# Kernel optimization log

Measured on AMD Instinct MI355X. Metric: run time of the kernel, lower is better.

## Reference

```python
import jax, jax.numpy as jnp
import numpy as np

N = 20000       # nodes
E = 262144      # edges
DA, DV, DD = 128, 64, 32
R = 16          # CP rank of TensorProds
NRAD = 8        # radial basis size (hardcoded 8 in module)
R0 = 5.0        # cutoff radius r0


def setup_inputs() -> dict:
    key = jax.random.key(0)
    ks = jax.random.split(key, 13)
    nrm = lambda k, shape, fan: jax.random.normal(k, shape, jnp.float32) / np.sqrt(fan)
    return {
        'r_ij': jax.random.normal(ks[0], (E, 3), jnp.float32),
        'x_a': jax.random.normal(ks[1], (N, DA), jnp.float32),
        'x_v': jax.random.normal(ks[2], (N, DV, 3), jnp.float32),
        'x_d': jax.random.normal(ks[3], (N, DD, 3, 3), jnp.float32),
        'W1_a': nrm(ks[4], (3, R, DA), DA),   # tp_000, tp_011, tp_022 (rank-0 input)
        'W1_v': nrm(ks[5], (4, R, DV), DV),   # tp_101, tp_110, tp_112, tp_121
        'W1_d': nrm(ks[6], (4, R, DD), DD),   # tp_202, tp_211, tp_220, tp_222
        'W2': nrm(ks[7], (11, R, NRAD), NRAD),  # radial-side proj for all 11 TPs
        'Wo_a': nrm(ks[8], (3, DA, R), R),    # outputs of tp_000, tp_110, tp_220
        'Wo_v': nrm(ks[9], (4, DV, R), R),    # outputs of tp_011, tp_101, tp_121, tp_211
        'Wo_d': nrm(ks[10], (4, DD, R), R),   # outputs of tp_022, tp_112, tp_202, tp_222
        'src': jax.random.randint(ks[11], (E,), 0, N),
        'dst': jax.random.randint(ks[12], (E,), 0, N),
    }


def tens_sigmoid_vec(v, eps=1e-6):
    # direction-preserving bounded nonlinearity on rank-1 tensors
    n = jnp.linalg.norm(v, axis=-1, keepdims=True)
    return v * (2.0 * jax.nn.sigmoid(n) - 1.0) / (n + eps)


def _forward(r_ij, x_a, x_v, x_d, W1_a, W1_v, W1_d, W2, Wo_a, Wo_v, Wo_d, src, dst):
    n_nodes = x_a.shape[0]
    # radial_encode_edge(r, 8, r0)
    npi = jnp.pi * jnp.arange(NRAD, dtype=jnp.float32)
    x_sq = jnp.sum(r_ij * r_ij, -1) / R0                       # (E,)
    rad = jnp.cos(npi * jnp.sqrt(x_sq)[:, None]) * jax.nn.relu(1.0 - x_sq)[:, None]  # (E,8)
    rv = tens_sigmoid_vec(r_ij * (17.0 / R0))                  # (E,3)
    phi_a = rad                                                # (E,8)
    phi_v = rad[..., None] * rv[:, None, :]                    # (E,8,3)
    phi_d = rad[..., None, None] * rv[:, None, None, :] * rv[:, None, :, None]  # (E,8,3,3)
    # edges_read_dst: gather node features at destination nodes
    xa_j, xv_j, xd_j = x_a[dst], x_v[dst], x_d[dst]
    p1 = lambda W, x: jnp.einsum('rc,ec...->er...', W, x)      # channel->CP-rank proj
    outp = lambda Wo, t: jnp.einsum('dr,er...->ed...', Wo, t)  # CP-rank->channel proj
    p2a = lambda i: jnp.einsum('rc,ec->er', W2[i], phi_a)
    p2v = lambda i: jnp.einsum('rc,eci->eri', W2[i], phi_v)
    p2d = lambda i: jnp.einsum('rc,ecij->erij', W2[i], phi_d)
    # W2 index order: 000,110,220,011,101,121,211,022,112,202,222
    pa000, pa011, pa022 = p1(W1_a[0], xa_j), p1(W1_a[1], xa_j), p1(W1_a[2], xa_j)
    pv101, pv110, pv112, pv121 = (p1(W1_v[i], xv_j) for i in range(4))
    pd202, pd211, pd220, pd222 = (p1(W1_d[i], xd_j) for i in range(4))
    psi_a = (outp(Wo_a[0], pa000 * p2a(0))
             + outp(Wo_a[1], jnp.einsum('eri,eri->er', pv110, p2v(1)))
             + outp(Wo_a[2], jnp.einsum('erij,erij->er', pd220, p2d(2))))
    psi_v = (outp(Wo_v[0], pa011[..., None] * p2v(3))
             + outp(Wo_v[1], pv101 * p2a(4)[..., None])
             + outp(Wo_v[2], jnp.einsum('eri,erij->erj', pv121, p2d(5)))
             + outp(Wo_v[3], jnp.einsum('erij,erj->eri', pd211, p2v(6))))
    psi_d = (outp(Wo_d[0], pa022[..., None, None] * p2d(7))
             + outp(Wo_d[1], jnp.einsum('eri,erj->erij', pv112, p2v(8)))
             + outp(Wo_d[2], pd202 * p2a(9)[..., None, None])
             + outp(Wo_d[3], jnp.einsum('erik,erkj->erij', pd222, p2d(10))))
    # edges_reduce_src: scatter-add messages to source nodes
    B_a = jax.ops.segment_sum(psi_a, src, num_segments=n_nodes)
    B_v = jax.ops.segment_sum(psi_v, src, num_segments=n_nodes)
    B_d = jax.ops.segment_sum(psi_d, src, num_segments=n_nodes)
    return (B_a, B_v, B_d)


def reference(r_ij, x_a, x_v, x_d, W1_a, W1_v, W1_d, W2, Wo_a, Wo_v, Wo_d, src, dst):
    return _forward(r_ij, x_a, x_v, x_d, W1_a, W1_v, W1_d, W2, Wo_a, Wo_v, Wo_d, src, dst)
```

## Files before the change

kernel.cpp:

```cpp
#include <hip/hip_runtime.h>
#include <hip/hip_bf16.h>
#include <math.h>

#define PI_F 3.14159265358979323846f
#define R0_F 5.0f


static __device__ __forceinline__ float dot4(float4 a, float4 b) {
  return a.x * b.x + a.y * b.y + a.z * b.z + a.w * b.w;
}

__global__ __launch_bounds__(256) void node_proj_kernel(
    const float* __restrict__ x_a, const float* __restrict__ x_v, const float* __restrict__ x_d,
    const float* __restrict__ W1_a, const float* __restrict__ W1_v, const float* __restrict__ W1_d,
    float* __restrict__ P, int N)
{
  __shared__ float S[12352];
  const int tid = threadIdx.x;
  const int lane = tid & 63;
  const int wu = __builtin_amdgcn_readfirstlane(tid >> 6);
  const int n0 = blockIdx.x * 64;
  const int nrem = min(N - n0, 64);
  const int phase = blockIdx.y;

  if (phase == 0) {
    for (int idx4 = tid; idx4 < nrem * 32; idx4 += 256) {
      int n = idx4 >> 5, c4 = idx4 & 31;
      float4 v = ((const float4*)(x_a + (size_t)(n0 + n) * 128))[c4];
      float* d = &S[n * 129 + c4 * 4];
      d[0] = v.x; d[1] = v.y; d[2] = v.z; d[3] = v.w;
    }
    __syncthreads();
    float acc[12];
    #pragma unroll
    for (int q = 0; q < 12; q++) acc[q] = 0.0f;
    const float* xrow = &S[lane * 129];
    for (int c0 = 0; c0 < 128; c0 += 16) {
      float xr[16];
      #pragma unroll
      for (int j = 0; j < 16; j++) xr[j] = xrow[c0 + j];
      #pragma unroll
      for (int q = 0; q < 12; q++) {
        int o = wu * 12 + q;
        const float* wp = W1_a + (o >> 4) * 2048 + (o & 15) * 128 + c0;
        float s = 0.0f;
        #pragma unroll
        for (int j = 0; j < 16; j++) s += wp[j] * xr[j];
        acc[q] += s;
      }
    }
    __syncthreads();
    #pragma unroll
    for (int q = 0; q < 12; q++) S[lane * 49 + wu * 12 + q] = acc[q];
    __syncthreads();
    for (int u = tid; u < nrem * 12; u += 256) {
      int n = u / 12, m4 = u - n * 12;
      const float* s = &S[n * 49 + m4 * 4];
      ((float4*)(P + (size_t)(n0 + n) * 816))[m4] = make_float4(s[0], s[1], s[2], s[3]);
    }
  } else if (phase == 1) {
    for (int idx4 = tid; idx4 < nrem * 48; idx4 += 256) {
      int n = idx4 / 48, m4 = idx4 - n * 48;
      float4 v = ((const float4*)(x_v + (size_t)(n0 + n) * 192))[m4];
      float* d = &S[n * 193 + m4 * 4];
      d[0] = v.x; d[1] = v.y; d[2] = v.z; d[3] = v.w;
    }
    __syncthreads();
    float acc[16][3];
    #pragma unroll
    for (int r = 0; r < 16; r++)
      #pragma unroll
      for (int i = 0; i < 3; i++) acc[r][i] = 0.0f;
    const float* xrow = &S[lane * 193];
    for (int c0 = 0; c0 < 64; c0 += 16) {
      float xr[16][3];
      #pragma unroll
      for (int j = 0; j < 16; j++) {
        xr[j][0] = xrow[(c0 + j) * 3 + 0];
        xr[j][1] = xrow[(c0 + j) * 3 + 1];
        xr[j][2] = xrow[(c0 + j) * 3 + 2];
      }
      #pragma unroll
      for (int r = 0; r < 16; r++) {
        const float* wp = W1_v + wu * 1024 + r * 64 + c0;
        #pragma unroll
        for (int j = 0; j < 16; j++) {
          float w = wp[j];
          acc[r][0] += w * xr[j][0];
          acc[r][1] += w * xr[j][1];
          acc[r][2] += w * xr[j][2];
        }
      }
    }
    __syncthreads();
    #pragma unroll
    for (int r = 0; r < 16; r++)
      #pragma unroll
      for (int i = 0; i < 3; i++)
        S[lane * 193 + wu * 48 + r * 3 + i] = acc[r][i];
    __syncthreads();
    for (int u = tid; u < nrem * 48; u += 256) {
      int n = u / 48, m4 = u - n * 48;
      const float* s = &S[n * 193 + m4 * 4];
      ((float4*)(P + (size_t)(n0 + n) * 816 + 48))[m4] = make_float4(s[0], s[1], s[2], s[3]);
    }
  } else if (phase == 2) {
    for (int idx = tid; idx < nrem * 160; idx += 256) {
      int n = idx / 160, m = idx - n * 160, c = m / 5, ij = m - c * 5;
      S[n * 161 + m] = x_d[(size_t)(n0 + n) * 288 + c * 9 + ij];
    }
    __syncthreads();
    float acc[16][5];
    #pragma unroll
    for (int r = 0; r < 16; r++)
      #pragma unroll
      for (int t = 0; t < 5; t++) acc[r][t] = 0.0f;
    const float* xrow = &S[lane * 161];
    for (int c0 = 0; c0 < 32; c0 += 8) {
      float xr[8][5];
      #pragma unroll
      for (int j = 0; j < 8; j++)
        #pragma unroll
        for (int t = 0; t < 5; t++) xr[j][t] = xrow[(c0 + j) * 5 + t];
      #pragma unroll
      for (int r = 0; r < 16; r++) {
        const float* wp = W1_d + wu * 512 + r * 32 + c0;
        #pragma unroll
        for (int j = 0; j < 8; j++) {
          float w = wp[j];
          #pragma unroll
          for (int t = 0; t < 5; t++) acc[r][t] += w * xr[j][t];
        }
      }
    }
    #pragma unroll
    for (int h = 0; h < 2; h++) {
      __syncthreads();
      if ((lane >> 5) == h) {
        int l5 = lane & 31;
        #pragma unroll
        for (int r = 0; r < 16; r++)
          #pragma unroll
          for (int t = 0; t < 5; t++)
            S[l5 * 321 + wu * 80 + r * 5 + t] = acc[r][t];
      }
      __syncthreads();
      int nbase = h * 32;
      int cnt = min(nrem - nbase, 32);
      for (int u = tid; u < cnt * 320; u += 256) {
        int n = u / 320, m = u - n * 320;
        int kk = m / 80, mm = m - kk * 80, rr = mm / 5, t = mm - rr * 5;
        P[(size_t)(n0 + nbase + n) * 816 + 240 + kk * 144 + 9 * rr + t] = S[n * 321 + m];
      }
    }
  } else {
    for (int idx = tid; idx < nrem * 128; idx += 256) {
      int n = idx >> 7, m = idx & 127, c = m >> 2, t = m & 3;
      S[n * 129 + m] = x_d[(size_t)(n0 + n) * 288 + c * 9 + 5 + t];
    }
    __syncthreads();
    float acc[16][4];
    #pragma unroll
    for (int r = 0; r < 16; r++)
      #pragma unroll
      for (int t = 0; t < 4; t++) acc[r][t] = 0.0f;
    const float* xrow = &S[lane * 129];
    for (int c0 = 0; c0 < 32; c0 += 8) {
      float xr[8][4];
      #pragma unroll
      for (int j = 0; j < 8; j++)
        #pragma unroll
        for (int t = 0; t < 4; t++) xr[j][t] = xrow[(c0 + j) * 4 + t];
      #pragma unroll
      for (int r = 0; r < 16; r++) {
        const float* wp = W1_d + wu * 512 + r * 32 + c0;
        #pragma unroll
        for (int j = 0; j < 8; j++) {
          float w = wp[j];
          #pragma unroll
          for (int t = 0; t < 4; t++) acc[r][t] += w * xr[j][t];
        }
      }
    }
    #pragma unroll
    for (int h = 0; h < 2; h++) {
      __syncthreads();
      if ((lane >> 5) == h) {
        int l5 = lane & 31;
        #pragma unroll
        for (int r = 0; r < 16; r++)
          #pragma unroll
          for (int t = 0; t < 4; t++)
            S[l5 * 257 + wu * 64 + r * 4 + t] = acc[r][t];
      }
      __syncthreads();
      int nbase = h * 32;
      int cnt = min(nrem - nbase, 32);
      for (int u = tid; u < cnt * 256; u += 256) {
        int n = u >> 8, m = u & 255;
        int kk = m >> 6, mm = m & 63, rr = mm >> 2, t = mm & 3;
        P[(size_t)(n0 + nbase + n) * 816 + 240 + kk * 144 + 9 * rr + 5 + t] = S[n * 257 + m];
      }
    }
  }
}

__global__ void hist_kernel(const int* __restrict__ src, int* __restrict__ counts, int E) {
  int e = blockIdx.x * 256 + threadIdx.x;
  if (e < E) atomicAdd(&counts[src[e]], 1);
}

__global__ __launch_bounds__(1024) void scan_kernel(
    const int* __restrict__ counts, int* __restrict__ offs, int* __restrict__ cursor,
    int N, int E)
{
  __shared__ int part[1024];
  int tid = threadIdx.x;
  int chunk = (N + 1023) / 1024;
  int lo = tid * chunk, hi = min(lo + chunk, N);
  int s = 0;
  for (int i = lo; i < hi; i++) s += counts[i];
  part[tid] = s;
  __syncthreads();
  for (int off = 1; off < 1024; off <<= 1) {
    int v = (tid >= off) ? part[tid - off] : 0;
    __syncthreads();
    part[tid] += v;
    __syncthreads();
  }
  int run = part[tid] - s;
  for (int i = lo; i < hi; i++) { offs[i] = run; cursor[i] = run; run += counts[i]; }
  if (tid == 0) offs[N] = E;
}

__global__ void scatter_kernel(const int* __restrict__ src, int* __restrict__ cursor,
                               int* __restrict__ eidx, int E) {
  int e = blockIdx.x * 256 + threadIdx.x;
  if (e < E) { int p = atomicAdd(&cursor[src[e]], 1); eidx[p] = e; }
}

__global__ __launch_bounds__(256) void node_gather_kernel(
    const float* __restrict__ r_ij, const int* __restrict__ dst,
    const int* __restrict__ offs, const int* __restrict__ eidx,
    const float* __restrict__ Pg, const float* __restrict__ W2,
    const float* __restrict__ Wo_a, const float* __restrict__ Wo_v, const float* __restrict__ Wo_d,
    float* __restrict__ out, int N)
{
  __shared__ __align__(16) float Sall[7488];
  const int wid = threadIdx.x >> 6;
  const int lane = threadIdx.x & 63;
  const int n = blockIdx.x * 4 + wid;
  if (n >= N) return;
  float* S = Sall + wid * 1872;
  float4* S4 = (float4*)S;
  int* Si = (int*)S;
  const int off = offs[n], deg = offs[n + 1] - off;

  int aP[12], aQ[12], aF[12];
  unsigned typm = 0;
  #pragma unroll
  for (int p = 0; p < 3; p++) {
    int t = lane + 64 * p;
    int k = t / 48, m = t - 48 * k, jj = m >> 4, r = m & 15;
    int q_ = 816 + (3 + k) * 16 + r;
    int P_, F_;
    if (k == 0)      { P_ = 16 + r;              F_ = 992 + jj; }
    else if (k == 1) { P_ = 48 + 3 * r + jj;     F_ = 995; }
    else if (k == 2) { P_ = 192 + 3 * r;         F_ = 992 + jj; typm |= 1u << p; }
    else             { P_ = 384 + 9 * r + 3 * jj; F_ = 995;     typm |= 1u << p; }
    aP[p] = P_; aQ[p] = q_; aF[p] = F_;
  }
  #pragma unroll
  for (int p = 0; p < 9; p++) {
    int u = lane + 64 * p;
    int s = u / 144, m = u - 144 * s, ij = m >> 4, r = m & 15;
    int i = ij / 3, jj = ij - 3 * i;
    int P_, F_, q_;
    if (s == 0)      { P_ = 32 + r;              q_ = 112 + r; F_ = 996 + ij; }
    else if (s == 1) { P_ = 144 + 3 * r + i;     q_ = 128 + r; F_ = 992 + jj; }
    else if (s == 2) { P_ = 240 + 9 * r + ij;    q_ = 144 + r; F_ = 995; }
    else             { P_ = 672 + 9 * r + 3 * i; q_ = 160 + r; F_ = 992 + jj; typm |= 1u << (3 + p); }
    aP[3 + p] = P_; aQ[3 + p] = 816 + q_; aF[3 + p] = F_;
  }
  const int ak = lane >> 4, ar = lane & 15;

  float4 wqa[3], wqb[3];
  #pragma unroll
  for (int p = 0; p < 3; p++) {
    int tq = lane + 64 * p; if (tq > 175) tq = 175;
    const float4* w = (const float4*)(W2 + tq * 8);
    wqa[p] = w[0]; wqb[p] = w[1];
  }

  float accA = 0.0f, acc[12];
  #pragma unroll
  for (int p = 0; p < 12; p++) acc[p] = 0.0f;

  float4 pb0 = {}, pb1 = {}, pb2 = {}, pb3 = {};
  const int l3 = 192 + (lane < 12 ? lane : 0);

  for (int base = 0; base < deg; base += 64) {
    const int cnt = min(deg - base, 64);
    bool live = false;
    float a = 0, b = 0, c = 0;
    int d = 0;
    if (lane < cnt) {
      int e = eidx[off + base + lane];
      a = r_ij[3 * (size_t)e]; b = r_ij[3 * (size_t)e + 1]; c = r_ij[3 * (size_t)e + 2];
      d = dst[e];
      live = (a * a + b * b + c * c) < 5.0f;
    }
    unsigned long long mb = __ballot(live);
    const int cl = __popcll(mb);
    if (live) {
      int pos = __popcll(mb & ((1ull << lane) - 1ull));
      float rr = a * a + b * b + c * c;
      float x_sq = rr * (1.0f / R0_F);
      float env = 1.0f - x_sq;
      float v0 = a * (17.0f / R0_F), v1 = b * (17.0f / R0_F), v2 = c * (17.0f / R0_F);
      float nn = sqrtf(v0 * v0 + v1 * v1 + v2 * v2);
      float sig = 2.0f / (1.0f + __expf(-nn)) - 1.0f;
      float scs = sig / (nn + 1e-6f);
      float rv0 = v0 * scs, rv1 = v1 * scs, rv2 = v2 * scs;
      float c1 = __cosf(PI_F * sqrtf(x_sq));
      float two_c1 = 2.0f * c1, cm2 = 1.0f, cm1 = c1;
      float rad[8];
      rad[0] = env; rad[1] = c1 * env;
      #pragma unroll
      for (int k = 2; k < 8; k++) { float cc = two_c1 * cm1 - cm2; rad[k] = cc * env; cm2 = cm1; cm1 = cc; }
      Si[1008 + pos] = d;
      S4[268 + 3 * pos]     = make_float4(rv0, rv1, rv2, 0.0f);
      S4[268 + 3 * pos + 1] = make_float4(rad[0], rad[1], rad[2], rad[3]);
      S4[268 + 3 * pos + 2] = make_float4(rad[4], rad[5], rad[6], rad[7]);
    }
    if (cl == 0) continue;
    {
      int d0 = Si[1008];
      const float4* Pp = (const float4*)(Pg + (size_t)d0 * 816);
      pb0 = Pp[lane]; pb1 = Pp[64 + lane]; pb2 = Pp[128 + lane]; pb3 = Pp[l3];
      S4[lane] = pb0; S4[64 + lane] = pb1; S4[128 + lane] = pb2;
      if (lane < 12) S4[192 + lane] = pb3;
      float4 s1 = S4[269], s2 = S4[270];
      S[816 + lane] = dot4(wqa[0], s1) + dot4(wqb[0], s2);
      S[880 + lane] = dot4(wqa[1], s1) + dot4(wqb[1], s2);
      if (lane < 48) S[944 + lane] = dot4(wqa[2], s1) + dot4(wqb[2], s2);
      float4 s0 = S4[268];
      if (lane < 13) {
        float tv;
        if (lane < 4) tv = (lane == 0) ? s0.x : (lane == 1) ? s0.y : (lane == 2) ? s0.z : 1.0f;
        else { int ij_ = lane - 4, i_ = ij_ / 3, j_ = ij_ - 3 * i_;
               float av = (i_ == 0) ? s0.x : (i_ == 1) ? s0.y : s0.z;
               float bv = (j_ == 0) ? s0.x : (j_ == 1) ? s0.y : s0.z;
               tv = av * bv; }
        S[992 + lane] = tv;
      }
      if (cl > 1) {
        int d1 = Si[1009];
        const float4* Pq = (const float4*)(Pg + (size_t)d1 * 816);
        pb0 = Pq[lane]; pb1 = Pq[64 + lane]; pb2 = Pq[128 + lane]; pb3 = Pq[l3];
      }
    }
    for (int t = 0; t < cl; t++) {
      float4 sc0 = S4[268 + 3 * t];
      float rv0 = sc0.x, rv1 = sc0.y, rv2 = sc0.z;
      if (lane < 48) {
        float v;
        if (ak == 0)      v = S[ar] * S[816 + ar];
        else if (ak == 1) v = (S[96 + 3 * ar] * rv0 + S[97 + 3 * ar] * rv1 + S[98 + 3 * ar] * rv2) * S[832 + ar];
        else {
          int bb = 528 + 9 * ar;
          float o = (S[bb] * rv0 + S[bb + 3] * rv1 + S[bb + 6] * rv2) * rv0
                  + (S[bb + 1] * rv0 + S[bb + 4] * rv1 + S[bb + 7] * rv2) * rv1
                  + (S[bb + 2] * rv0 + S[bb + 5] * rv1 + S[bb + 8] * rv2) * rv2;
          v = o * S[848 + ar];
        }
        accA += v;
      }
      #pragma unroll
      for (int p = 0; p < 12; p++) {
        float pv;
        if (typm & (1u << p)) pv = S[aP[p]] * rv0 + S[aP[p] + 1] * rv1 + S[aP[p] + 2] * rv2;
        else                  pv = S[aP[p]];
        acc[p] += pv * S[aQ[p]] * S[aF[p]];
      }
      if (t + 1 < cl) {
        S4[lane] = pb0; S4[64 + lane] = pb1; S4[128 + lane] = pb2;
        if (lane < 12) S4[192 + lane] = pb3;
        float4 s1 = S4[268 + 3 * (t + 1) + 1], s2 = S4[268 + 3 * (t + 1) + 2];
        S[816 + lane] = dot4(wqa[0], s1) + dot4(wqb[0], s2);
        S[880 + lane] = dot4(wqa[1], s1) + dot4(wqb[1], s2);
        if (lane < 48) S[944 + lane] = dot4(wqa[2], s1) + dot4(wqb[2], s2);
        float4 nx0 = S4[268 + 3 * (t + 1)];
        if (lane < 13) {
          float tv;
          if (lane < 4) tv = (lane == 0) ? nx0.x : (lane == 1) ? nx0.y : (lane == 2) ? nx0.z : 1.0f;
          else { int ij_ = lane - 4, i_ = ij_ / 3, j_ = ij_ - 3 * i_;
                 float av = (i_ == 0) ? nx0.x : (i_ == 1) ? nx0.y : nx0.z;
                 float bv = (j_ == 0) ? nx0.x : (j_ == 1) ? nx0.y : nx0.z;
                 tv = av * bv; }
          S[992 + lane] = tv;
        }
      }
      if (t + 2 < cl) {
        int d2 = Si[1008 + t + 2];
        const float4* Pp = (const float4*)(Pg + (size_t)d2 * 816);
        pb0 = Pp[lane]; pb1 = Pp[64 + lane]; pb2 = Pp[128 + lane]; pb3 = Pp[l3];
      }
    }
  }

  if (lane < 48) S[lane] = accA;
  #pragma unroll
  for (int p = 0; p < 3; p++) S[48 + lane + 64 * p] = acc[p];
  #pragma unroll
  for (int p = 0; p < 9; p++) {
    int u = lane + 64 * p;
    int s = u / 144, m = u - 144 * s, ij = m >> 4, r = m & 15;
    S[240 + s * 180 + ij * 20 + r] = acc[3 + p];
  }

  const size_t baseV = (size_t)N * 128;
  const size_t baseD = (size_t)N * 320;

  #pragma unroll
  for (int h = 0; h < 2; h++) {
    int c = lane + 64 * h;
    float a_ = 0.0f;
    #pragma unroll
    for (int k = 0; k < 3; k++) {
      const float4* w = (const float4*)(Wo_a + k * 2048 + c * 16);
      const float4* A4 = (const float4*)(&S[k * 16]);
      #pragma unroll
      for (int cc = 0; cc < 4; cc++) a_ += dot4(w[cc], A4[cc]);
    }
    out[(size_t)n * 128 + c] = a_;
  }
  {
    float o0 = 0, o1 = 0, o2 = 0;
    #pragma unroll
    for (int k = 0; k < 4; k++) {
      const float4* w = (const float4*)(Wo_v + k * 1024 + lane * 16);
      float4 w0 = w[0], w1 = w[1], w2 = w[2], w3 = w[3];
      #pragma unroll
      for (int j = 0; j < 3; j++) {
        const float4* A4 = (const float4*)(&S[48 + k * 48 + j * 16]);
        float v = dot4(w0, A4[0]) + dot4(w1, A4[1]) + dot4(w2, A4[2]) + dot4(w3, A4[3]);
        if (j == 0) o0 += v; else if (j == 1) o1 += v; else o2 += v;
      }
    }
    size_t ov = baseV + (size_t)n * 192 + lane * 3;
    out[ov] = o0; out[ov + 1] = o1; out[ov + 2] = o2;
  }
  #pragma unroll
  for (int p = 0; p < 5; p++) {
    int t = lane + 64 * p;
    if (t < 288) {
      int d = t / 9, ij = t - 9 * d;
      float a_ = 0.0f;
      #pragma unroll
      for (int s = 0; s < 4; s++) {
        const float4* w = (const float4*)(Wo_d + s * 512 + d * 16);
        const float4* A4 = (const float4*)(&S[240 + s * 180 + ij * 20]);
        a_ += dot4(w[0], A4[0]) + dot4(w[1], A4[1]) + dot4(w[2], A4[2]) + dot4(w[3], A4[3]);
      }
      out[baseD + (size_t)n * 288 + t] = a_;
    }
  }
}

extern "C" void kernel_launch(void* const* d_in, const int* in_sizes, int n_in,
                              void* d_out, int out_size, void* d_ws, size_t ws_size,
                              hipStream_t stream) {
  const float* r_ij = (const float*)d_in[0];
  const float* x_a  = (const float*)d_in[1];
  const float* x_v  = (const float*)d_in[2];
  const float* x_d  = (const float*)d_in[3];
  const float* W1_a = (const float*)d_in[4];
  const float* W1_v = (const float*)d_in[5];
  const float* W1_d = (const float*)d_in[6];
  const float* W2   = (const float*)d_in[7];
  const float* Wo_a = (const float*)d_in[8];
  const float* Wo_v = (const float*)d_in[9];
  const float* Wo_d = (const float*)d_in[10];
  const int*  src   = (const int*)d_in[11];
  const int*  dst   = (const int*)d_in[12];

  const int E = in_sizes[0] / 3;
  const int N = in_sizes[1] / 128;

  float* P    = (float*)d_ws;
  int* counts = (int*)(P + (size_t)N * 816);
  int* offs   = counts + N;
  int* cursor = offs + N + 1;
  int* eidx   = cursor + N;

  hipMemsetAsync(counts, 0, sizeof(int) * (size_t)N, stream);

  hist_kernel<<<(E + 255) / 256, 256, 0, stream>>>(src, counts, E);
  scan_kernel<<<1, 1024, 0, stream>>>(counts, offs, cursor, N, E);
  scatter_kernel<<<(E + 255) / 256, 256, 0, stream>>>(src, cursor, eidx, E);
  dim3 g1((N + 63) / 64, 4);
  node_proj_kernel<<<g1, 256, 0, stream>>>(x_a, x_v, x_d, W1_a, W1_v, W1_d, P, N);
  node_gather_kernel<<<(N + 3) / 4, 256, 0, stream>>>(r_ij, dst, offs, eidx, P, W2,
                                                      Wo_a, Wo_v, Wo_d, (float*)d_out, N);
}
```

Measured before the change: 456.7 us.

## Relayout node projections per lane group and compute edge messages in registers

Node projection outputs are rewritten into a lane-group-major layout, so each 16-lane group of a wave loads its 13 per-rank values with strided scalar loads straight into registers. The gather kernel drops the per-edge shared-memory staging of the projection row and of the radial/outer-product factors. Each lane now computes its own radial weights and accumulates dedicated tensor components, with two register buffers holding alternate edges so prefetch runs ahead. This cuts LDS traffic and barrier-like serialization per edge, at the cost of uncoalesced strided global loads and extra divergent per-group branches.

```diff
diff --git a/kernel.cpp b/kernel.cpp
--- a/kernel.cpp
+++ b/kernel.cpp
@@ -53,10 +53,10 @@
     #pragma unroll
     for (int q = 0; q < 12; q++) S[lane * 49 + wu * 12 + q] = acc[q];
     __syncthreads();
-    for (int u = tid; u < nrem * 12; u += 256) {
-      int n = u / 12, m4 = u - n * 12;
-      const float* s = &S[n * 49 + m4 * 4];
-      ((float4*)(P + (size_t)(n0 + n) * 816))[m4] = make_float4(s[0], s[1], s[2], s[3]);
+    for (int u = tid; u < nrem * 48; u += 256) {
+      int n = u / 48, m = u - n * 48, k = m >> 4, r = m & 15;
+      int gA = (k == 0) ? 0 : (k == 1) ? 208 : 416;
+      P[(size_t)(n0 + n) * 816 + gA + 192 + r] = S[n * 49 + m];
     }
   } else if (phase == 1) {
     for (int idx4 = tid; idx4 < nrem * 48; idx4 += 256) {
@@ -99,10 +99,11 @@
       for (int i = 0; i < 3; i++)
         S[lane * 193 + wu * 48 + r * 3 + i] = acc[r][i];
     __syncthreads();
-    for (int u = tid; u < nrem * 48; u += 256) {
-      int n = u / 48, m4 = u - n * 48;
-      const float* s = &S[n * 193 + m4 * 4];
-      ((float4*)(P + (size_t)(n0 + n) * 816 + 48))[m4] = make_float4(s[0], s[1], s[2], s[3]);
+    for (int u = tid; u < nrem * 192; u += 256) {
+      int n = u / 192, m = u - n * 192;
+      int k = m / 48, mm = m - k * 48, r = mm / 3, i = mm - r * 3;
+      int gV = (k == 0) ? 208 : (k == 1) ? 0 : (k == 2) ? 624 : 416;
+      P[(size_t)(n0 + n) * 816 + gV + 144 + i * 16 + r] = S[n * 193 + m];
     }
   } else if (phase == 2) {
     for (int idx = tid; idx < nrem * 160; idx += 256) {
@@ -149,8 +150,9 @@
       int cnt = min(nrem - nbase, 32);
       for (int u = tid; u < cnt * 320; u += 256) {
         int n = u / 320, m = u - n * 320;
-        int kk = m / 80, mm = m - kk * 80, rr = mm / 5, t = mm - rr * 5;
-        P[(size_t)(n0 + nbase + n) * 816 + 240 + kk * 144 + 9 * rr + t] = S[n * 321 + m];
+        int k = m / 80, mm = m - k * 80, r = mm / 5, t = mm - r * 5;
+        int gD = (k == 0) ? 208 : (k == 1) ? 416 : (k == 2) ? 624 : 0;
+        P[(size_t)(n0 + nbase + n) * 816 + gD + t * 16 + r] = S[n * 321 + m];
       }
     }
   } else {
@@ -198,8 +200,9 @@
       int cnt = min(nrem - nbase, 32);
       for (int u = tid; u < cnt * 256; u += 256) {
         int n = u >> 8, m = u & 255;
-        int kk = m >> 6, mm = m & 63, rr = mm >> 2, t = mm & 3;
-        P[(size_t)(n0 + nbase + n) * 816 + 240 + kk * 144 + 9 * rr + 5 + t] = S[n * 257 + m];
+        int k = m >> 6, mm = m & 63, r = mm >> 2, t = mm & 3;
+        int gD = (k == 0) ? 208 : (k == 1) ? 416 : (k == 2) ? 624 : 0;
+        P[(size_t)(n0 + nbase + n) * 816 + gD + (5 + t) * 16 + r] = S[n * 257 + m];
       }
     }
   }
@@ -239,6 +242,60 @@
   if (e < E) { int p = atomicAdd(&cursor[src[e]], 1); eidx[p] = e; }
 }
 
+#define EDGE_BODY(T, PC)                                                       \
+  {                                                                            \
+    const int t_ = (T);                                                        \
+    float4 rvv = S4[240 + 3 * t_];                                             \
+    float4 ra_ = S4[240 + 3 * t_ + 1];                                         \
+    float4 rb_ = S4[240 + 3 * t_ + 2];                                         \
+    float q0 = dot4(w0a, ra_) + dot4(w0b, rb_);                                \
+    float q1 = dot4(w1a, ra_) + dot4(w1b, rb_);                                \
+    float q2 = dot4(w2a, ra_) + dot4(w2b, rb_);                                \
+    float rv0 = rvv.x, rv1 = rvv.y, rv2 = rvv.z;                               \
+    if (g == 0) {                                                              \
+      float t0 = PC[0] * rv0 + PC[1] * rv1 + PC[2] * rv2;                      \
+      float t1 = PC[3] * rv0 + PC[4] * rv1 + PC[5] * rv2;                      \
+      float t2 = PC[6] * rv0 + PC[7] * rv1 + PC[8] * rv2;                      \
+      float u0 = q0 * t0, u1 = q0 * t1, u2 = q0 * t2;                          \
+      accD[0] += u0 * rv0; accD[1] += u0 * rv1; accD[2] += u0 * rv2;           \
+      accD[3] += u1 * rv0; accD[4] += u1 * rv1; accD[5] += u1 * rv2;           \
+      accD[6] += u2 * rv0; accD[7] += u2 * rv1; accD[8] += u2 * rv2;           \
+      accS += q1 * (PC[9] * rv0 + PC[10] * rv1 + PC[11] * rv2);                \
+      accT += q2 * PC[12];                                                     \
+    } else if (g == 1) {                                                       \
+      _Pragma("unroll")                                                        \
+      for (int j = 0; j < 9; j++) accD[j] += q0 * PC[j];                       \
+      accV[0] += q1 * PC[9]; accV[1] += q1 * PC[10]; accV[2] += q1 * PC[11];   \
+      float o = q2 * PC[12];                                                   \
+      accW[0] += o * rv0; accW[1] += o * rv1; accW[2] += o * rv2;              \
+    } else if (g == 2) {                                                       \
+      accV[0] += q0 * (PC[0] * rv0 + PC[1] * rv1 + PC[2] * rv2);               \
+      accV[1] += q0 * (PC[3] * rv0 + PC[4] * rv1 + PC[5] * rv2);               \
+      accV[2] += q0 * (PC[6] * rv0 + PC[7] * rv1 + PC[8] * rv2);               \
+      float s_ = q1 * (PC[9] * rv0 + PC[10] * rv1 + PC[11] * rv2);             \
+      accW[0] += s_ * rv0; accW[1] += s_ * rv1; accW[2] += s_ * rv2;           \
+      float o = q2 * PC[12];                                                   \
+      float o0 = o * rv0, o1 = o * rv1, o2 = o * rv2;                          \
+      accD[0] += o0 * rv0; accD[1] += o0 * rv1; accD[2] += o0 * rv2;           \
+      accD[3] += o1 * rv0; accD[4] += o1 * rv1; accD[5] += o1 * rv2;           \
+      accD[6] += o2 * rv0; accD[7] += o2 * rv1; accD[8] += o2 * rv2;           \
+    } else {                                                                   \
+      float t0 = PC[0] * rv0 + PC[1] * rv1 + PC[2] * rv2;                      \
+      float t1 = PC[3] * rv0 + PC[4] * rv1 + PC[5] * rv2;                      \
+      float t2 = PC[6] * rv0 + PC[7] * rv1 + PC[8] * rv2;                      \
+      accS += q0 * (t0 * rv0 + t1 * rv1 + t2 * rv2);                           \
+      float m0 = q1 * PC[9], m1 = q1 * PC[10], m2 = q1 * PC[11];               \
+      accD[0] += m0 * rv0; accD[1] += m0 * rv1; accD[2] += m0 * rv2;           \
+      accD[3] += m1 * rv0; accD[4] += m1 * rv1; accD[5] += m1 * rv2;           \
+      accD[6] += m2 * rv0; accD[7] += m2 * rv1; accD[8] += m2 * rv2;           \
+    }                                                                          \
+    if (t_ + 2 < cl) {                                                         \
+      const float* bp = PbaseG + (size_t)Si[1728 + t_ + 2] * 816;              \
+      _Pragma("unroll")                                                        \
+      for (int j = 0; j < 13; j++) PC[j] = bp[j * 16];                         \
+    }                                                                          \
+  }
+
 __global__ __launch_bounds__(256) void node_gather_kernel(
     const float* __restrict__ r_ij, const int* __restrict__ dst,
     const int* __restrict__ offs, const int* __restrict__ eidx,
@@ -246,58 +303,38 @@
     const float* __restrict__ Wo_a, const float* __restrict__ Wo_v, const float* __restrict__ Wo_d,
     float* __restrict__ out, int N)
 {
-  __shared__ __align__(16) float Sall[7488];
+  __shared__ __align__(16) float Sall[7168];
   const int wid = threadIdx.x >> 6;
   const int lane = threadIdx.x & 63;
   const int n = blockIdx.x * 4 + wid;
   if (n >= N) return;
-  float* S = Sall + wid * 1872;
+  float* S = Sall + wid * 1792;
   float4* S4 = (float4*)S;
   int* Si = (int*)S;
   const int off = offs[n], deg = offs[n + 1] - off;
-
-  int aP[12], aQ[12], aF[12];
-  unsigned typm = 0;
+  const int g = lane >> 4, r = lane & 15;
+  const int gbase = (g == 0) ? 0 : (g == 1) ? 208 : (g == 2) ? 416 : 624;
+  const float* PbaseG = Pg + gbase + r;
+
+  int i0, i1, i2;
+  if (g == 0)      { i0 = 10; i1 = 1; i2 = 0; }
+  else if (g == 1) { i0 = 9;  i1 = 4; i2 = 3; }
+  else if (g == 2) { i0 = 6;  i1 = 5; i2 = 7; }
+  else             { i0 = 2;  i1 = 8; i2 = 8; }
+  const float4* w2p0 = (const float4*)(W2 + (i0 * 16 + r) * 8);
+  const float4* w2p1 = (const float4*)(W2 + (i1 * 16 + r) * 8);
+  const float4* w2p2 = (const float4*)(W2 + (i2 * 16 + r) * 8);
+  float4 w0a = w2p0[0], w0b = w2p0[1];
+  float4 w1a = w2p1[0], w1b = w2p1[1];
+  float4 w2a = w2p2[0], w2b = w2p2[1];
+
+  float accD[9], accV[3], accW[3], accS = 0.0f, accT = 0.0f;
   #pragma unroll
-  for (int p = 0; p < 3; p++) {
-    int t = lane + 64 * p;
-    int k = t / 48, m = t - 48 * k, jj = m >> 4, r = m & 15;
-    int q_ = 816 + (3 + k) * 16 + r;
-    int P_, F_;
-    if (k == 0)      { P_ = 16 + r;              F_ = 992 + jj; }
-    else if (k == 1) { P_ = 48 + 3 * r + jj;     F_ = 995; }
-    else if (k == 2) { P_ = 192 + 3 * r;         F_ = 992 + jj; typm |= 1u << p; }
-    else             { P_ = 384 + 9 * r + 3 * jj; F_ = 995;     typm |= 1u << p; }
-    aP[p] = P_; aQ[p] = q_; aF[p] = F_;
-  }
+  for (int j = 0; j < 9; j++) accD[j] = 0.0f;
   #pragma unroll
-  for (int p = 0; p < 9; p++) {
-    int u = lane + 64 * p;
-    int s = u / 144, m = u - 144 * s, ij = m >> 4, r = m & 15;
-    int i = ij / 3, jj = ij - 3 * i;
-    int P_, F_, q_;
-    if (s == 0)      { P_ = 32 + r;              q_ = 112 + r; F_ = 996 + ij; }
-    else if (s == 1) { P_ = 144 + 3 * r + i;     q_ = 128 + r; F_ = 992 + jj; }
-    else if (s == 2) { P_ = 240 + 9 * r + ij;    q_ = 144 + r; F_ = 995; }
-    else             { P_ = 672 + 9 * r + 3 * i; q_ = 160 + r; F_ = 992 + jj; typm |= 1u << (3 + p); }
-    aP[3 + p] = P_; aQ[3 + p] = 816 + q_; aF[3 + p] = F_;
-  }
-  const int ak = lane >> 4, ar = lane & 15;
-
-  float4 wqa[3], wqb[3];
-  #pragma unroll
-  for (int p = 0; p < 3; p++) {
-    int tq = lane + 64 * p; if (tq > 175) tq = 175;
-    const float4* w = (const float4*)(W2 + tq * 8);
-    wqa[p] = w[0]; wqb[p] = w[1];
-  }
-
-  float accA = 0.0f, acc[12];
-  #pragma unroll
-  for (int p = 0; p < 12; p++) acc[p] = 0.0f;
-
-  float4 pb0 = {}, pb1 = {}, pb2 = {}, pb3 = {};
-  const int l3 = 192 + (lane < 12 ? lane : 0);
+  for (int j = 0; j < 3; j++) { accV[j] = 0.0f; accW[j] = 0.0f; }
+
+  float PA[13], PB[13];
 
   for (int base = 0; base < deg; base += 64) {
     const int cnt = min(deg - base, 64);
@@ -328,95 +365,55 @@
       rad[0] = env; rad[1] = c1 * env;
       #pragma unroll
       for (int k = 2; k < 8; k++) { float cc = two_c1 * cm1 - cm2; rad[k] = cc * env; cm2 = cm1; cm1 = cc; }
-      Si[1008 + pos] = d;
-      S4[268 + 3 * pos]     = make_float4(rv0, rv1, rv2, 0.0f);
-      S4[268 + 3 * pos + 1] = make_float4(rad[0], rad[1], rad[2], rad[3]);
-      S4[268 + 3 * pos + 2] = make_float4(rad[4], rad[5], rad[6], rad[7]);
+      Si[1728 + pos] = d;
+      S4[240 + 3 * pos]     = make_float4(rv0, rv1, rv2, 0.0f);
+      S4[240 + 3 * pos + 1] = make_float4(rad[0], rad[1], rad[2], rad[3]);
+      S4[240 + 3 * pos + 2] = make_float4(rad[4], rad[5], rad[6], rad[7]);
     }
     if (cl == 0) continue;
     {
-      int d0 = Si[1008];
-      const float4* Pp = (const float4*)(Pg + (size_t)d0 * 816);
-      pb0 = Pp[lane]; pb1 = Pp[64 + lane]; pb2 = Pp[128 + lane]; pb3 = Pp[l3];
-      S4[lane] = pb0; S4[64 + lane] = pb1; S4[128 + lane] = pb2;
-      if (lane < 12) S4[192 + lane] = pb3;
-      float4 s1 = S4[269], s2 = S4[270];
-      S[816 + lane] = dot4(wqa[0], s1) + dot4(wqb[0], s2);
-      S[880 + lane] = dot4(wqa[1], s1) + dot4(wqb[1], s2);
-      if (lane < 48) S[944 + lane] = dot4(wqa[2], s1) + dot4(wqb[2], s2);
-      float4 s0 = S4[268];
-      if (lane < 13) {
-        float tv;
-        if (lane < 4) tv = (lane == 0) ? s0.x : (lane == 1) ? s0.y : (lane == 2) ? s0.z : 1.0f;
-        else { int ij_ = lane - 4, i_ = ij_ / 3, j_ = ij_ - 3 * i_;
-               float av = (i_ == 0) ? s0.x : (i_ == 1) ? s0.y : s0.z;
-               float bv = (j_ == 0) ? s0.x : (j_ == 1) ? s0.y : s0.z;
-               tv = av * bv; }
-        S[992 + lane] = tv;
-      }
+      const float* bp = PbaseG + (size_t)Si[1728] * 816;
+      #pragma unroll
+      for (int j = 0; j < 13; j++) PA[j] = bp[j * 16];
       if (cl > 1) {
-        int d1 = Si[1009];
-        const float4* Pq = (const float4*)(Pg + (size_t)d1 * 816);
-        pb0 = Pq[lane]; pb1 = Pq[64 + lane]; pb2 = Pq[128 + lane]; pb3 = Pq[l3];
-      }
-    }
-    for (int t = 0; t < cl; t++) {
-      float4 sc0 = S4[268 + 3 * t];
-      float rv0 = sc0.x, rv1 = sc0.y, rv2 = sc0.z;
-      if (lane < 48) {
-        float v;
-        if (ak == 0)      v = S[ar] * S[816 + ar];
-        else if (ak == 1) v = (S[96 + 3 * ar] * rv0 + S[97 + 3 * ar] * rv1 + S[98 + 3 * ar] * rv2) * S[832 + ar];
-        else {
-          int bb = 528 + 9 * ar;
-          float o = (S[bb] * rv0 + S[bb + 3] * rv1 + S[bb + 6] * rv2) * rv0
-                  + (S[bb + 1] * rv0 + S[bb + 4] * rv1 + S[bb + 7] * rv2) * rv1
-                  + (S[bb + 2] * rv0 + S[bb + 5] * rv1 + S[bb + 8] * rv2) * rv2;
-          v = o * S[848 + ar];
-        }
-        accA += v;
-      }
-      #pragma unroll
-      for (int p = 0; p < 12; p++) {
-        float pv;
-        if (typm & (1u << p)) pv = S[aP[p]] * rv0 + S[aP[p] + 1] * rv1 + S[aP[p] + 2] * rv2;
-        else                  pv = S[aP[p]];
-        acc[p] += pv * S[aQ[p]] * S[aF[p]];
-      }
+        const float* bq = PbaseG + (size_t)Si[1729] * 816;
+        #pragma unroll
+        for (int j = 0; j < 13; j++) PB[j] = bq[j * 16];
+      }
+    }
+    for (int t = 0; t < cl; t += 2) {
+      EDGE_BODY(t, PA)
       if (t + 1 < cl) {
-        S4[lane] = pb0; S4[64 + lane] = pb1; S4[128 + lane] = pb2;
-        if (lane < 12) S4[192 + lane] = pb3;
-        float4 s1 = S4[268 + 3 * (t + 1) + 1], s2 = S4[268 + 3 * (t + 1) + 2];
-        S[816 + lane] = dot4(wqa[0], s1) + dot4(wqb[0], s2);
-        S[880 + lane] = dot4(wqa[1], s1) + dot4(wqb[1], s2);
-        if (lane < 48) S[944 + lane] = dot4(wqa[2], s1) + dot4(wqb[2], s2);
-        float4 nx0 = S4[268 + 3 * (t + 1)];
-        if (lane < 13) {
-          float tv;
-          if (lane < 4) tv = (lane == 0) ? nx0.x : (lane == 1) ? nx0.y : (lane == 2) ? nx0.z : 1.0f;
-          else { int ij_ = lane - 4, i_ = ij_ / 3, j_ = ij_ - 3 * i_;
-                 float av = (i_ == 0) ? nx0.x : (i_ == 1) ? nx0.y : nx0.z;
-                 float bv = (j_ == 0) ? nx0.x : (j_ == 1) ? nx0.y : nx0.z;
-                 tv = av * bv; }
-          S[992 + lane] = tv;
-        }
-      }
-      if (t + 2 < cl) {
-        int d2 = Si[1008 + t + 2];
-        const float4* Pp = (const float4*)(Pg + (size_t)d2 * 816);
-        pb0 = Pp[lane]; pb1 = Pp[64 + lane]; pb2 = Pp[128 + lane]; pb3 = Pp[l3];
-      }
-    }
-  }
-
-  if (lane < 48) S[lane] = accA;
-  #pragma unroll
-  for (int p = 0; p < 3; p++) S[48 + lane + 64 * p] = acc[p];
-  #pragma unroll
-  for (int p = 0; p < 9; p++) {
-    int u = lane + 64 * p;
-    int s = u / 144, m = u - 144 * s, ij = m >> 4, r = m & 15;
-    S[240 + s * 180 + ij * 20 + r] = acc[3 + p];
+        EDGE_BODY(t + 1, PB)
+      }
+    }
+  }
+
+  if (g == 0) {
+    S[r] = accT;
+    S[16 + r] = accS;
+    #pragma unroll
+    for (int ij = 0; ij < 9; ij++) S[240 + 540 + ij * 20 + r] = accD[ij];
+  } else if (g == 1) {
+    #pragma unroll
+    for (int j = 0; j < 3; j++) {
+      S[48 + j * 16 + r] = accW[j];
+      S[96 + j * 16 + r] = accV[j];
+    }
+    #pragma unroll
+    for (int ij = 0; ij < 9; ij++) S[240 + 360 + ij * 20 + r] = accD[ij];
+  } else if (g == 2) {
+    #pragma unroll
+    for (int j = 0; j < 3; j++) {
+      S[144 + j * 16 + r] = accW[j];
+      S[192 + j * 16 + r] = accV[j];
+    }
+    #pragma unroll
+    for (int ij = 0; ij < 9; ij++) S[240 + ij * 20 + r] = accD[ij];
+  } else {
+    S[32 + r] = accS;
+    #pragma unroll
+    for (int ij = 0; ij < 9; ij++) S[240 + 180 + ij * 20 + r] = accD[ij];
   }
 
   const size_t baseV = (size_t)N * 128;
```

After: 395.0 us. 1.16x faster.
